# Optimization experiments

Hardware: AMD Instinct MI355X
Metric: run time of the kernel (lower is better)

## Reference

```python
import jax, jax.numpy as jnp
import numpy as np

M = N = 768
Q = 32
P_ROW = P_COL = 4
NB_ITER = 3


def cheb_basis(L, order):
    # Chebyshev polynomials T_k(L), stacked -> (order+1, n, n)
    n = L.shape[0]
    Ts = [jnp.eye(n, dtype=L.dtype)]
    if order > 0:
        Ts.append(L)
    for _ in range(2, order + 1):
        Ts.append(2.0 * (L @ Ts[-1]) - Ts[-2])
    return jnp.stack(Ts)


def setup_inputs() -> dict:
    key = jax.random.key(0)
    ks = jax.random.split(key, 24)
    f32 = jnp.float32
    # scaled symmetric Laplacians with small spectral radius (keeps Cheb recursion stable)
    Ar = jax.random.normal(ks[0], (M, M), dtype=f32)
    L_row = (Ar + Ar.T) / (2.0 * jnp.sqrt(jnp.float32(M)))
    Ac = jax.random.normal(ks[1], (N, N), dtype=f32)
    L_col = (Ac + Ac.T) / (2.0 * jnp.sqrt(jnp.float32(N)))
    x = jax.random.normal(ks[2], (M, N), dtype=f32)
    theta = 0.05 * jax.random.normal(ks[3], (P_ROW + 1, P_COL + 1, Q), dtype=f32)
    bias = jnp.zeros((Q,), dtype=f32)
    s = 1.0 / np.sqrt(Q)
    def w(k):
        return s * jax.random.normal(k, (Q, Q), dtype=f32)
    inp = {
        'x': x, 'L_row': L_row, 'L_col': L_col, 'theta': theta, 'bias': bias,
        'W_f': w(ks[4]), 'U_f': w(ks[5]), 'b_f': jnp.zeros((Q,), f32),
        'W_i': w(ks[6]), 'U_i': w(ks[7]), 'b_i': jnp.zeros((Q,), f32),
        'W_o': w(ks[8]), 'U_o': w(ks[9]), 'b_o': jnp.zeros((Q,), f32),
        'W_c': w(ks[10]), 'U_c': w(ks[11]), 'b_c': jnp.zeros((Q,), f32),
        'W_out': s * jax.random.normal(ks[12], (Q, 1), dtype=f32),
        'b_out': jnp.zeros((1, 1), f32),
        'nb_iterations_rnn': NB_ITER,
    }
    return inp


def reference(x, L_row, L_col, theta, bias,
              W_f, U_f, b_f, W_i, U_i, b_i, W_o, U_o, b_o, W_c, U_c, b_c,
              W_out, b_out, nb_iterations_rnn):
    pr = theta.shape[0] - 1
    pc = theta.shape[1] - 1
    q = theta.shape[2]
    m, n = x.shape
    Tr = cheb_basis(L_row, pr)  # (pr+1, M, M)
    Tc = cheb_basis(L_col, pc)  # (pc+1, N, N)

    def conv(xx):
        xr = jnp.einsum('imp,pn->imn', Tr, xx)            # (pr+1, M, N)
        bf = jnp.einsum('imn,jnk->ijmk', xr, Tc)           # (pr+1, pc+1, M, N)
        return jnp.einsum('ijmn,ijo->omn', bf, theta) + bias[:, None, None]

    def step(carry, _):
        xx, h, c = carry
        xc = conv(xx).transpose(1, 2, 0).reshape(-1, q)    # (M*N, q)
        f = jax.nn.sigmoid(xc @ W_f + h @ U_f + b_f)
        i = jax.nn.sigmoid(xc @ W_i + h @ U_i + b_i)
        o = jax.nn.sigmoid(xc @ W_o + h @ U_o + b_o)
        cu = jax.nn.sigmoid(xc @ W_c + h @ U_c + b_c)      # note: sigmoid, as in source
        c = f * c + i * cu
        h = o * jax.nn.sigmoid(c)                           # note: sigmoid(c), as in source
        dx = jnp.tanh(c @ W_out + b_out).reshape(m, n)
        return (xx + dx, h, c), None

    h0 = jnp.zeros((m * n, q), dtype=x.dtype)
    c0 = jnp.zeros((m * n, q), dtype=x.dtype)
    (x_out, _, _), _ = jax.lax.scan(step, (x, h0, c0), None, length=int(nb_iterations_rnn))
    return x_out
```

## Files before the change

kernel.cpp:

```cpp
#include <hip/hip_runtime.h>
#include <hip/hip_bf16.h>
#include <stdint.h>


#define DIM 768
#define MXK 589824
#define STK 2949120

typedef _Float16 f16x8 __attribute__((ext_vector_type(8)));
typedef float f32x4 __attribute__((ext_vector_type(4)));
typedef unsigned short ushort_t;
typedef _Float16 f16_t;

__device__ __forceinline__ float sigm(float v) {
    float e = __expf(-v);
    return __builtin_amdgcn_rcpf(1.0f + e);
}
__device__ __forceinline__ void split2h(float f, f16_t& h1, f16_t& h2) {
    h1 = (f16_t)f;
    h2 = (f16_t)(f - (float)h1);
}

__device__ __forceinline__ void gl_lds16(const f16_t* g, f16_t* l) {
    auto gp = reinterpret_cast<const __attribute__((address_space(1))) uint32_t*>(
        reinterpret_cast<uintptr_t>(g));
    auto lp = reinterpret_cast<__attribute__((address_space(3))) uint32_t*>(
        reinterpret_cast<uintptr_t>(l));
    __builtin_amdgcn_global_load_lds(gp, lp, 16, 0, 0);
}

__global__ __launch_bounds__(256) void init_split(
    const float* __restrict__ Lrow, const float* __restrict__ Lcol,
    f16_t* __restrict__ S0, f16_t* __restrict__ S1)
{
    int idx = blockIdx.x * 256 + threadIdx.x;
    int p = idx / DIM, m = idx % DIM;
    f16_t eye = (p == m) ? (f16_t)1.0f : (f16_t)0.0f;
    S0[idx] = eye; S1[idx] = (f16_t)0.0f;
    S0[STK + idx] = eye; S1[STK + idx] = (f16_t)0.0f;
    f16_t h1, h2;
    split2h(Lrow[idx], h1, h2);
    S0[MXK + idx] = h1; S1[MXK + idx] = h2;
    split2h(Lcol[idx], h1, h2);
    S0[STK + MXK + idx] = h1; S1[STK + MXK + idx] = h2;
}

__global__ __launch_bounds__(256) void prep_gate(
    const float* __restrict__ Wf, const float* __restrict__ Wi,
    const float* __restrict__ Wo, const float* __restrict__ Wc,
    const float* __restrict__ Uf, const float* __restrict__ Ui,
    const float* __restrict__ Uo, const float* __restrict__ Uc,
    const float* __restrict__ theta, const float* __restrict__ biasv,
    f16_t* __restrict__ Wstack, f16_t* __restrict__ thstack)
{
    int idx = blockIdx.x * 256 + threadIdx.x;
    if (idx < 8192) {
        int R = idx >> 6, k = idx & 63;
        int g = (R >> 4) & 3, o = (R >> 6) * 16 + (R & 15);
        const float* Wg[4] = {Wf, Wi, Wo, Wc};
        const float* Ug[4] = {Uf, Ui, Uo, Uc};
        float v = (k < 32) ? Wg[g][k * 32 + o] : Ug[g][(k - 32) * 32 + o];
        Wstack[idx] = (f16_t)v;
    } else if (idx < 9216) {
        int t = idx - 8192;
        int o = t >> 5, k = t & 31;
        float v = (k < 25) ? theta[k * 32 + o]
                           : (k == 25 ? biasv[o] : 0.0f);
        thstack[o * 32 + k] = (f16_t)v;
    }
}

__global__ __launch_bounds__(256) void transpose_cvt2x(
    const float* __restrict__ in, f16_t* __restrict__ o1,
    f16_t* __restrict__ o2, f16_t* __restrict__ xr0,
    f16_t* __restrict__ Cbf)
{
    __shared__ float t[32][33];
    int x = threadIdx.x & 31, y = threadIdx.x >> 5;
    int bx = blockIdx.x * 32, by = blockIdx.y * 32;
#pragma unroll
    for (int r = 0; r < 4; ++r) {
        int p = by + y + 8 * r, q = bx + x;
        size_t oi = (size_t)p * DIM + q;
        float v = in[oi];
        t[y + 8 * r][x] = v;
        f16_t hv = (f16_t)v;
        xr0[oi] = hv;
        Cbf[(size_t)p * 3840 + q] = hv;
    }
    __syncthreads();
#pragma unroll
    for (int r = 0; r < 4; ++r) {
        float v = t[x][y + 8 * r];
        f16_t h1, h2;
        split2h(v, h1, h2);
        size_t o = (size_t)(bx + y + 8 * r) * DIM + by + x;
        o1[o] = h1; o2[o] = h2;
    }
}

__global__ __launch_bounds__(256, 4) void gemm_bt_h2(
    const f16_t* __restrict__ A1,
    const f16_t* __restrict__ B1, const f16_t* __restrict__ B2,
    const f16_t* __restrict__ P1, const f16_t* __restrict__ P2,
    f16_t* __restrict__ D1, f16_t* __restrict__ D2, f16_t* __restrict__ D3,
    int K, int ldc, int mode, int nbx, int halfStride, int coloff)
{
    __shared__ __align__(16) f16_t sA[2][128 * 32];
    __shared__ __align__(16) f16_t sB[2][2 * 96 * 32];

    const int tid = threadIdx.x;

    int bx, by;
    size_t hoff = 0;
    int aoff = 0, boff = 0, poff = 0, doff = 0;
    if (mode == 3) {
        int g = blockIdx.x;
        int sup = g >> 8;
        int rows0 = sup * 8;
        int H = 30 - rows0; if (H > 8) H = 8;
        int local = g - rows0 * nbx;
        by = rows0 + local % H;
        bx = local / H;
    } else if (mode == 4) {
        int g = blockIdx.x;
        int t34 = g / 96, r = g % 96;
        int stack = r / 48, rr = r % 48;
        by = rr >> 3; bx = rr & 7;
        hoff = (size_t)stack * halfStride;
        if (t34 == 0) { aoff = MXK; boff = 2 * MXK; poff = MXK; doff = 3 * MXK; }
        else          { aoff = 2 * MXK; boff = 2 * MXK; poff = 0; doff = 4 * MXK; }
    } else {
        bx = blockIdx.x % nbx;
        by = blockIdx.x / nbx;
        if (mode == 2 && by >= 6) { by -= 6; hoff = (size_t)halfStride; }
    }
    const int m0 = by * 128, n0 = bx * 96;

    const f16_t* Asrc1 = A1 + hoff + aoff;
    const f16_t* Bsrc1 = B1 + hoff + boff;
    const f16_t* Bsrc2 = B2 + hoff + boff;
    const f16_t* Pq1 = P1 ? P1 + hoff + poff : nullptr;
    const f16_t* Pq2 = P2 ? P2 + hoff + poff : nullptr;
    f16_t* Dq1 = D1 + hoff + doff;
    f16_t* Dq2 = D2 ? D2 + hoff + doff : nullptr;

    const int lane = tid & 63, w4 = tid >> 6;
    const int wm = (w4 & 1) * 64, wn = (w4 >> 1) * 48;
    const int lm = lane & 15, quad = lane >> 4;
    const int psw = (quad ^ ((lm >> 1) & 3)) * 8;

    const f16_t* gApt[2]; int aslot[2];
#pragma unroll
    for (int cc = 0; cc < 2; ++cc) {
        int s = cc * 256 + w4 * 64 + lane;
        int row = s >> 2, pos = s & 3;
        int chunk = pos ^ ((row >> 1) & 3);
        gApt[cc] = Asrc1 + (size_t)(m0 + row) * K + chunk * 8;
        aslot[cc] = s * 8;
    }
    const f16_t* gBpt[3]; int bslot[3];
#pragma unroll
    for (int cc = 0; cc < 3; ++cc) {
        int slot = cc * 256 + w4 * 64 + lane;
        int lev = slot >= 384 ? 1 : 0;
        int s = slot - lev * 384;
        int row = s >> 2, pos = s & 3;
        int chunk = pos ^ ((row >> 1) & 3);
        gBpt[cc] = (lev ? Bsrc2 : Bsrc1) + (size_t)(n0 + row) * K + chunk * 8;
        bslot[cc] = lev * 3072 + s * 8;
    }

    f32x4 acc[4][3] = {};

#pragma unroll
    for (int cc = 0; cc < 2; ++cc) gl_lds16(gApt[cc], &sA[0][aslot[cc]]);
#pragma unroll
    for (int cc = 0; cc < 3; ++cc) gl_lds16(gBpt[cc], &sB[0][bslot[cc]]);
    __syncthreads();

    int ib = 0;
    for (int kb = 0; kb < K; kb += 32, ib ^= 1) {
        if (kb + 32 < K) {
            int nb = ib ^ 1;
#pragma unroll
            for (int cc = 0; cc < 2; ++cc)
                gl_lds16(gApt[cc] + kb + 32, &sA[nb][aslot[cc]]);
#pragma unroll
            for (int cc = 0; cc < 3; ++cc)
                gl_lds16(gBpt[cc] + kb + 32, &sB[nb][bslot[cc]]);
        }

        f16x8 bfr[2][3];
#pragma unroll
        for (int l = 0; l < 2; ++l)
#pragma unroll
            for (int fn = 0; fn < 3; ++fn)
                bfr[l][fn] = *(const f16x8*)&sB[ib][l * 3072 +
                                                (wn + fn * 16 + lm) * 32 + psw];
#pragma unroll
        for (int fm = 0; fm < 4; ++fm) {
            f16x8 a1v = *(const f16x8*)&sA[ib][(wm + fm * 16 + lm) * 32 + psw];
#pragma unroll
            for (int fn = 0; fn < 3; ++fn) {
                acc[fm][fn] = __builtin_amdgcn_mfma_f32_16x16x32_f16(
                    a1v, bfr[0][fn], acc[fm][fn], 0, 0, 0);
                acc[fm][fn] = __builtin_amdgcn_mfma_f32_16x16x32_f16(
                    a1v, bfr[1][fn], acc[fm][fn], 0, 0, 0);
            }
        }
        __syncthreads();
    }

#pragma unroll
    for (int fm = 0; fm < 4; ++fm)
#pragma unroll
        for (int fn = 0; fn < 3; ++fn) {
            int col = n0 + wn + fn * 16 + lm;
#pragma unroll
            for (int r = 0; r < 4; ++r) {
                int row = m0 + wm + fm * 16 + quad * 4 + r;
                float val = acc[fm][fn][r];
                if (mode == 3) {
                    Dq1[(size_t)row * ldc + coloff + col] = (f16_t)val;
                } else if (mode == 1) {
                    Dq1[(size_t)row * ldc + col] = (f16_t)val;
                    if (D3) D3[(size_t)row * 3840 + col] = (f16_t)val;
                } else {
                    size_t o = (size_t)row * ldc + col;
                    val = 2.0f * val - ((float)Pq1[o] + (float)Pq2[o]);
                    f16_t h1, h2;
                    split2h(val, h1, h2);
                    Dq1[o] = h1; Dq2[o] = h2;
                }
            }
        }
}

__global__ __launch_bounds__(256, 4) void gate_theta_mfma(
    const f16_t* __restrict__ Cbf, const f16_t* __restrict__ thstack,
    const f16_t* __restrict__ Wstack,
    const float* __restrict__ bfv, const float* __restrict__ biv,
    const float* __restrict__ bov, const float* __restrict__ bcv,
    const float* __restrict__ Wout, const float* __restrict__ bout,
    f16_t* __restrict__ h, f16_t* __restrict__ c, float* __restrict__ x,
    int first, int last)
{
    __shared__ __align__(16) ushort_t sB[128 * 40];
    __shared__ __align__(16) ushort_t sC[26 * 128];
    __shared__ float red[256];

    const int tid = threadIdx.x;
    const int lane = tid & 63, w4 = tid >> 6;
    const int wm = (w4 & 1) * 64, wn = (w4 >> 1) * 64;
    const int lm = lane & 15, quad = lane >> 4;
    const int m = blockIdx.x / 6;
    const int n0 = (blockIdx.x % 6) * 128;
    const int pbase = m * DIM + n0;
    const int o0 = (wm >> 2) + quad * 4;

#pragma unroll
    for (int cc = 0; cc < 2; ++cc) {
        int s = cc * 256 + tid;
        if (s < 416) {
            int ij = s >> 4, f = s & 15;
            if (ij < 25) {
                int i5 = (ij * 205) >> 10;
                int j5 = ij - i5 * 5;
                size_t ga = (size_t)(i5 * DIM + m) * 3840 + j5 * DIM + n0 + f * 8;
                *(uint4*)&sC[ij * 128 + f * 8] = *(const uint4*)&Cbf[ga];
            } else {
                uint4 ones;
                ones.x = ones.y = ones.z = ones.w = 0x3C003C00u;
                *(uint4*)&sC[25 * 128 + f * 8] = ones;
            }
        }
    }

    f16x8 bth[2];
#pragma unroll
    for (int fn = 0; fn < 2; ++fn)
        bth[fn] = *(const f16x8*)&thstack[(fn * 16 + lm) * 32 + quad * 8];

    f16x8 hfr[4];
    f16_t cold[4][4];
    if (!first) {
#pragma unroll
        for (int fn = 0; fn < 4; ++fn) {
            size_t p = (size_t)(pbase + wn + fn * 16 + lm);
            hfr[fn] = *(const f16x8*)&h[p * 32 + quad * 8];
            *(uint2*)cold[fn] = *(const uint2*)&c[p * 32 + o0];
        }
    } else {
#pragma unroll
        for (int fn = 0; fn < 4; ++fn) {
#pragma unroll
            for (int j = 0; j < 8; ++j) hfr[fn][j] = (f16_t)0.0f;
#pragma unroll
            for (int r = 0; r < 4; ++r) cold[fn][r] = (f16_t)0.0f;
        }
    }

    __syncthreads();

    {
        const f16_t* sCf = (const f16_t*)sC;
        const int pw = w4 * 32;
        f32x4 tacc[2][2] = {};
        f16x8 a0, a1;
#pragma unroll
        for (int j = 0; j < 8; ++j) {
            int k = quad * 8 + j;
            int ij = k > 25 ? 25 : k;
            a0[j] = sCf[ij * 128 + pw + lm];
            a1[j] = sCf[ij * 128 + pw + 16 + lm];
        }
#pragma unroll
        for (int fn = 0; fn < 2; ++fn) {
            tacc[0][fn] = __builtin_amdgcn_mfma_f32_16x16x32_f16(
                a0, bth[fn], tacc[0][fn], 0, 0, 0);
            tacc[1][fn] = __builtin_amdgcn_mfma_f32_16x16x32_f16(
                a1, bth[fn], tacc[1][fn], 0, 0, 0);
        }
#pragma unroll
        for (int fm2 = 0; fm2 < 2; ++fm2)
#pragma unroll
            for (int fn = 0; fn < 2; ++fn)
#pragma unroll
                for (int r = 0; r < 4; ++r) {
                    f16_t hv = (f16_t)tacc[fm2][fn][r];
                    sB[(pw + fm2 * 16 + quad * 4 + r) * 40 + fn * 16 + lm] =
                        __builtin_bit_cast(ushort_t, hv);
                }
    }

    f16x8 af[4][2];
#pragma unroll
    for (int fm = 0; fm < 4; ++fm)
#pragma unroll
        for (int kc = 0; kc < 2; ++kc)
            af[fm][kc] = *(const f16x8*)&Wstack[(wm + fm * 16 + lm) * 64 +
                                                kc * 32 + quad * 8];
    __syncthreads();

    const float4 bgf = *(const float4*)&bfv[o0];
    const float4 bgi = *(const float4*)&biv[o0];
    const float4 bgo = *(const float4*)&bov[o0];
    const float4 bgc = *(const float4*)&bcv[o0];
    const float4 wo4 = *(const float4*)&Wout[o0];
    float bf4[4] = {bgf.x, bgf.y, bgf.z, bgf.w};
    float bi4[4] = {bgi.x, bgi.y, bgi.z, bgi.w};
    float bo4[4] = {bgo.x, bgo.y, bgo.z, bgo.w};
    float bc4[4] = {bgc.x, bgc.y, bgc.z, bgc.w};
    float wo[4] = {wo4.x, wo4.y, wo4.z, wo4.w};

#pragma unroll
    for (int fn = 0; fn < 4; ++fn) {
        f16x8 bxc = *(const f16x8*)&sB[(wn + fn * 16 + lm) * 40 + quad * 8];
        f32x4 acc[4] = {};
#pragma unroll
        for (int fm = 0; fm < 4; ++fm) {
            acc[fm] = __builtin_amdgcn_mfma_f32_16x16x32_f16(
                af[fm][0], bxc, acc[fm], 0, 0, 0);
            acc[fm] = __builtin_amdgcn_mfma_f32_16x16x32_f16(
                af[fm][1], hfr[fn], acc[fm], 0, 0, 0);
        }

        int px = wn + fn * 16 + lm;
        size_t p = (size_t)(pbase + px);
        f16_t cn16[4], hn16[4];
        float part = 0.f;
#pragma unroll
        for (int r = 0; r < 4; ++r) {
            float fg = sigm(acc[0][r] + bf4[r]);
            float ig = sigm(acc[1][r] + bi4[r]);
            float og = sigm(acc[2][r] + bo4[r]);
            float gg = sigm(acc[3][r] + bc4[r]);
            float cn = fg * (float)cold[fn][r] + ig * gg;
            cn16[r] = (f16_t)cn;
            hn16[r] = (f16_t)(og * sigm(cn));
            part = fmaf(cn, wo[r], part);
        }
        if (!last) {
            *(uint2*)&c[p * 32 + o0] = *(const uint2*)cn16;
            *(uint2*)&h[p * 32 + o0] = *(const uint2*)hn16;
        }
        part += __shfl_xor(part, 16, 64);
        part += __shfl_xor(part, 32, 64);
        if (quad == 0) red[px * 2 + (wm >> 6)] = part;
    }
    __syncthreads();
    if (tid < 128) {
        float v = red[tid * 2] + red[tid * 2 + 1] + bout[0];
        v = fminf(fmaxf(v, -15.f), 15.f);
        float e = __expf(2.f * v);
        x[pbase + tid] += (e - 1.f) * __builtin_amdgcn_rcpf(e + 1.f);
    }
}

extern "C" void kernel_launch(void* const* d_in, const int* in_sizes, int n_in,
                              void* d_out, int out_size, void* d_ws, size_t ws_size,
                              hipStream_t stream)
{
    const float* x_in  = (const float*)d_in[0];
    const float* Lrow  = (const float*)d_in[1];
    const float* Lcol  = (const float*)d_in[2];
    const float* theta = (const float*)d_in[3];
    const float* bias  = (const float*)d_in[4];
    const float* Wf = (const float*)d_in[5];
    const float* Uf = (const float*)d_in[6];
    const float* bf = (const float*)d_in[7];
    const float* Wi = (const float*)d_in[8];
    const float* Ui = (const float*)d_in[9];
    const float* bi = (const float*)d_in[10];
    const float* Wo = (const float*)d_in[11];
    const float* Uo = (const float*)d_in[12];
    const float* bo = (const float*)d_in[13];
    const float* Wc = (const float*)d_in[14];
    const float* Uc = (const float*)d_in[15];
    const float* bc = (const float*)d_in[16];
    const float* Wout = (const float*)d_in[17];
    const float* bout = (const float*)d_in[18];
    (void)in_sizes; (void)n_in; (void)out_size;

    float* out = (float*)d_out;

    f16_t* base = (f16_t*)d_ws;
    f16_t* Cbf  = base;
    f16_t* h    = Cbf + 14745600;
    f16_t* c    = h + 18874368;
    f16_t* S0   = c + 18874368;
    f16_t* S1   = S0 + 2 * STK;
    f16_t* XR0  = S1 + 2 * STK;
    f16_t* Wstack  = XR0 + STK;
    f16_t* thstack = Wstack + 8192;
    f16_t* xT0  = thstack + 1024;
    f16_t* xT1  = xT0 + MXK;
    if (ws_size < (size_t)136857600) return;

    hipMemcpyAsync(out, x_in, (size_t)MXK * 4, hipMemcpyDeviceToDevice, stream);

    prep_gate<<<36, 256, 0, stream>>>(Wf, Wi, Wo, Wc, Uf, Ui, Uo, Uc, theta,
                                      bias, Wstack, thstack);
    init_split<<<MXK / 256, 256, 0, stream>>>(Lrow, Lcol, S0, S1);
    gemm_bt_h2<<<96, 256, 0, stream>>>(
        S0 + MXK, S0 + MXK, S1 + MXK, S0, S1,
        S0 + 2 * MXK, S1 + 2 * MXK, nullptr,
        DIM, DIM, 2, 8, STK, 0);
    gemm_bt_h2<<<192, 256, 0, stream>>>(
        S0, S0, S1, S0, S1, S0, S1, nullptr,
        DIM, DIM, 4, 8, STK, 0);

    for (int it = 0; it < 3; ++it) {
        transpose_cvt2x<<<dim3(24, 24), 256, 0, stream>>>(out, xT0, xT1,
                                                          XR0, Cbf);
        gemm_bt_h2<<<192, 256, 0, stream>>>(
            S0 + MXK, xT0, xT1,
            nullptr, nullptr,
            XR0 + MXK, nullptr, Cbf + (size_t)DIM * 3840,
            DIM, DIM, 1, 8, 0, 0);
        gemm_bt_h2<<<960, 256, 0, stream>>>(
            XR0, S0 + STK + MXK, S1 + STK + MXK,
            nullptr, nullptr,
            Cbf, nullptr, nullptr, DIM, 3840, 3, 32, 0, DIM);
        gate_theta_mfma<<<4608, 256, 0, stream>>>(
            Cbf, thstack, Wstack,
            bf, bi, bo, bc, Wout, bout, h, c, out,
            it == 0 ? 1 : 0, it == 2 ? 1 : 0);
    }
}
```

Baseline: 509.4 us.

## Make gate kernel persistent per row with double-buffered async staging

```diff
diff --git a/kernel.cpp b/kernel.cpp
--- a/kernel.cpp
+++ b/kernel.cpp
@@ -237,7 +237,7 @@
         }
 }
 
-__global__ __launch_bounds__(256, 4) void gate_theta_mfma(
+__global__ __launch_bounds__(256, 3) void gate_theta_mfma(
     const f16_t* __restrict__ Cbf, const f16_t* __restrict__ thstack,
     const f16_t* __restrict__ Wstack,
     const float* __restrict__ bfv, const float* __restrict__ biv,
@@ -246,94 +246,42 @@
     f16_t* __restrict__ h, f16_t* __restrict__ c, float* __restrict__ x,
     int first, int last)
 {
-    __shared__ __align__(16) ushort_t sB[128 * 40];
-    __shared__ __align__(16) ushort_t sC[26 * 128];
+    __shared__ __align__(16) ushort_t sC[2][26 * 128];
+    __shared__ __align__(16) ushort_t sB[2][128 * 40];
     __shared__ float red[256];
 
     const int tid = threadIdx.x;
     const int lane = tid & 63, w4 = tid >> 6;
     const int wm = (w4 & 1) * 64, wn = (w4 >> 1) * 64;
     const int lm = lane & 15, quad = lane >> 4;
-    const int m = blockIdx.x / 6;
-    const int n0 = (blockIdx.x % 6) * 128;
-    const int pbase = m * DIM + n0;
+    const int m = blockIdx.x;
     const int o0 = (wm >> 2) + quad * 4;
-
-#pragma unroll
-    for (int cc = 0; cc < 2; ++cc) {
-        int s = cc * 256 + tid;
-        if (s < 416) {
-            int ij = s >> 4, f = s & 15;
-            if (ij < 25) {
+    const int pw = w4 * 32;
+
+    if (tid < 32) {
+        uint4 ones;
+        ones.x = ones.y = ones.z = ones.w = 0x3C003C00u;
+        *(uint4*)&sC[tid >> 4][25 * 128 + (tid & 15) * 8] = ones;
+    }
+
+    auto stage = [&](int n0, int buf) {
+#pragma unroll
+        for (int cc = 0; cc < 2; ++cc) {
+            int s = cc * 256 + tid;
+            if (s < 400) {
+                int ij = s >> 4, f = s & 15;
                 int i5 = (ij * 205) >> 10;
                 int j5 = ij - i5 * 5;
                 size_t ga = (size_t)(i5 * DIM + m) * 3840 + j5 * DIM + n0 + f * 8;
-                *(uint4*)&sC[ij * 128 + f * 8] = *(const uint4*)&Cbf[ga];
-            } else {
-                uint4 ones;
-                ones.x = ones.y = ones.z = ones.w = 0x3C003C00u;
-                *(uint4*)&sC[25 * 128 + f * 8] = ones;
-            }
-        }
-    }
+                gl_lds16(&Cbf[ga], (f16_t*)&sC[buf][ij * 128 + f * 8]);
+            }
+        }
+    };
 
     f16x8 bth[2];
 #pragma unroll
     for (int fn = 0; fn < 2; ++fn)
         bth[fn] = *(const f16x8*)&thstack[(fn * 16 + lm) * 32 + quad * 8];
-
-    f16x8 hfr[4];
-    f16_t cold[4][4];
-    if (!first) {
-#pragma unroll
-        for (int fn = 0; fn < 4; ++fn) {
-            size_t p = (size_t)(pbase + wn + fn * 16 + lm);
-            hfr[fn] = *(const f16x8*)&h[p * 32 + quad * 8];
-            *(uint2*)cold[fn] = *(const uint2*)&c[p * 32 + o0];
-        }
-    } else {
-#pragma unroll
-        for (int fn = 0; fn < 4; ++fn) {
-#pragma unroll
-            for (int j = 0; j < 8; ++j) hfr[fn][j] = (f16_t)0.0f;
-#pragma unroll
-            for (int r = 0; r < 4; ++r) cold[fn][r] = (f16_t)0.0f;
-        }
-    }
-
-    __syncthreads();
-
-    {
-        const f16_t* sCf = (const f16_t*)sC;
-        const int pw = w4 * 32;
-        f32x4 tacc[2][2] = {};
-        f16x8 a0, a1;
-#pragma unroll
-        for (int j = 0; j < 8; ++j) {
-            int k = quad * 8 + j;
-            int ij = k > 25 ? 25 : k;
-            a0[j] = sCf[ij * 128 + pw + lm];
-            a1[j] = sCf[ij * 128 + pw + 16 + lm];
-        }
-#pragma unroll
-        for (int fn = 0; fn < 2; ++fn) {
-            tacc[0][fn] = __builtin_amdgcn_mfma_f32_16x16x32_f16(
-                a0, bth[fn], tacc[0][fn], 0, 0, 0);
-            tacc[1][fn] = __builtin_amdgcn_mfma_f32_16x16x32_f16(
-                a1, bth[fn], tacc[1][fn], 0, 0, 0);
-        }
-#pragma unroll
-        for (int fm2 = 0; fm2 < 2; ++fm2)
-#pragma unroll
-            for (int fn = 0; fn < 2; ++fn)
-#pragma unroll
-                for (int r = 0; r < 4; ++r) {
-                    f16_t hv = (f16_t)tacc[fm2][fn][r];
-                    sB[(pw + fm2 * 16 + quad * 4 + r) * 40 + fn * 16 + lm] =
-                        __builtin_bit_cast(ushort_t, hv);
-                }
-    }
-
     f16x8 af[4][2];
 #pragma unroll
     for (int fm = 0; fm < 4; ++fm)
@@ -341,8 +289,6 @@
         for (int kc = 0; kc < 2; ++kc)
             af[fm][kc] = *(const f16x8*)&Wstack[(wm + fm * 16 + lm) * 64 +
                                                 kc * 32 + quad * 8];
-    __syncthreads();
-
     const float4 bgf = *(const float4*)&bfv[o0];
     const float4 bgi = *(const float4*)&biv[o0];
     const float4 bgo = *(const float4*)&bov[o0];
@@ -353,48 +299,136 @@
     float bo4[4] = {bgo.x, bgo.y, bgo.z, bgo.w};
     float bc4[4] = {bgc.x, bgc.y, bgc.z, bgc.w};
     float wo[4] = {wo4.x, wo4.y, wo4.z, wo4.w};
-
-#pragma unroll
-    for (int fn = 0; fn < 4; ++fn) {
-        f16x8 bxc = *(const f16x8*)&sB[(wn + fn * 16 + lm) * 40 + quad * 8];
-        f32x4 acc[4] = {};
-#pragma unroll
-        for (int fm = 0; fm < 4; ++fm) {
-            acc[fm] = __builtin_amdgcn_mfma_f32_16x16x32_f16(
-                af[fm][0], bxc, acc[fm], 0, 0, 0);
-            acc[fm] = __builtin_amdgcn_mfma_f32_16x16x32_f16(
-                af[fm][1], hfr[fn], acc[fm], 0, 0, 0);
-        }
-
-        int px = wn + fn * 16 + lm;
-        size_t p = (size_t)(pbase + px);
-        f16_t cn16[4], hn16[4];
-        float part = 0.f;
-#pragma unroll
-        for (int r = 0; r < 4; ++r) {
-            float fg = sigm(acc[0][r] + bf4[r]);
-            float ig = sigm(acc[1][r] + bi4[r]);
-            float og = sigm(acc[2][r] + bo4[r]);
-            float gg = sigm(acc[3][r] + bc4[r]);
-            float cn = fg * (float)cold[fn][r] + ig * gg;
-            cn16[r] = (f16_t)cn;
-            hn16[r] = (f16_t)(og * sigm(cn));
-            part = fmaf(cn, wo[r], part);
-        }
-        if (!last) {
-            *(uint2*)&c[p * 32 + o0] = *(const uint2*)cn16;
-            *(uint2*)&h[p * 32 + o0] = *(const uint2*)hn16;
-        }
-        part += __shfl_xor(part, 16, 64);
-        part += __shfl_xor(part, 32, 64);
-        if (quad == 0) red[px * 2 + (wm >> 6)] = part;
+    const float bout0 = bout[0];
+
+    stage(0, 0);
+    f16x8 hfr[4];
+    f16_t cold[4][4];
+    if (!first) {
+#pragma unroll
+        for (int fn = 0; fn < 4; ++fn) {
+            size_t p = (size_t)(m * DIM + wn + fn * 16 + lm);
+            hfr[fn] = *(const f16x8*)&h[p * 32 + quad * 8];
+            *(uint2*)cold[fn] = *(const uint2*)&c[p * 32 + o0];
+        }
+    } else {
+#pragma unroll
+        for (int fn = 0; fn < 4; ++fn) {
+#pragma unroll
+            for (int j = 0; j < 8; ++j) hfr[fn][j] = (f16_t)0.0f;
+#pragma unroll
+            for (int r = 0; r < 4; ++r) cold[fn][r] = (f16_t)0.0f;
+        }
     }
     __syncthreads();
-    if (tid < 128) {
-        float v = red[tid * 2] + red[tid * 2 + 1] + bout[0];
-        v = fminf(fmaxf(v, -15.f), 15.f);
-        float e = __expf(2.f * v);
-        x[pbase + tid] += (e - 1.f) * __builtin_amdgcn_rcpf(e + 1.f);
+
+    int tb = 0;
+    for (int t = 0; t < 6; ++t, tb ^= 1) {
+        const int n0 = t * 128;
+        const int pbase = m * DIM + n0;
+
+        {
+            const f16_t* sCf = (const f16_t*)sC[tb];
+            f32x4 tacc[2][2] = {};
+            f16x8 a0, a1;
+#pragma unroll
+            for (int j = 0; j < 8; ++j) {
+                int k = quad * 8 + j;
+                int ij = k > 25 ? 25 : k;
+                a0[j] = sCf[ij * 128 + pw + lm];
+                a1[j] = sCf[ij * 128 + pw + 16 + lm];
+            }
+#pragma unroll
+            for (int fn = 0; fn < 2; ++fn) {
+                tacc[0][fn] = __builtin_amdgcn_mfma_f32_16x16x32_f16(
+                    a0, bth[fn], tacc[0][fn], 0, 0, 0);
+                tacc[1][fn] = __builtin_amdgcn_mfma_f32_16x16x32_f16(
+                    a1, bth[fn], tacc[1][fn], 0, 0, 0);
+            }
+#pragma unroll
+            for (int fm2 = 0; fm2 < 2; ++fm2)
+#pragma unroll
+                for (int fn = 0; fn < 2; ++fn)
+#pragma unroll
+                    for (int r = 0; r < 4; ++r) {
+                        f16_t hv = (f16_t)tacc[fm2][fn][r];
+                        sB[tb][(pw + fm2 * 16 + quad * 4 + r) * 40 +
+                               fn * 16 + lm] = __builtin_bit_cast(ushort_t, hv);
+                    }
+        }
+        __syncthreads();
+
+        if (t < 5) stage(n0 + 128, tb ^ 1);
+        f16x8 hfrn[4];
+        f16_t coldn[4][4];
+        if (t < 5 && !first) {
+#pragma unroll
+            for (int fn = 0; fn < 4; ++fn) {
+                size_t p = (size_t)(pbase + 128 + wn + fn * 16 + lm);
+                hfrn[fn] = *(const f16x8*)&h[p * 32 + quad * 8];
+                *(uint2*)coldn[fn] = *(const uint2*)&c[p * 32 + o0];
+            }
+        } else {
+#pragma unroll
+            for (int fn = 0; fn < 4; ++fn) {
+#pragma unroll
+                for (int j = 0; j < 8; ++j) hfrn[fn][j] = (f16_t)0.0f;
+#pragma unroll
+                for (int r = 0; r < 4; ++r) coldn[fn][r] = (f16_t)0.0f;
+            }
+        }
+
+#pragma unroll
+        for (int fn = 0; fn < 4; ++fn) {
+            f16x8 bxc = *(const f16x8*)&sB[tb][(wn + fn * 16 + lm) * 40 +
+                                              quad * 8];
+            f32x4 acc[4] = {};
+#pragma unroll
+            for (int fm = 0; fm < 4; ++fm) {
+                acc[fm] = __builtin_amdgcn_mfma_f32_16x16x32_f16(
+                    af[fm][0], bxc, acc[fm], 0, 0, 0);
+                acc[fm] = __builtin_amdgcn_mfma_f32_16x16x32_f16(
+                    af[fm][1], hfr[fn], acc[fm], 0, 0, 0);
+            }
+
+            int px = wn + fn * 16 + lm;
+            size_t p = (size_t)(pbase + px);
+            f16_t cn16[4], hn16[4];
+            float part = 0.f;
+#pragma unroll
+            for (int r = 0; r < 4; ++r) {
+                float fg = sigm(acc[0][r] + bf4[r]);
+                float ig = sigm(acc[1][r] + bi4[r]);
+                float og = sigm(acc[2][r] + bo4[r]);
+                float gg = sigm(acc[3][r] + bc4[r]);
+                float cn = fg * (float)cold[fn][r] + ig * gg;
+                cn16[r] = (f16_t)cn;
+                hn16[r] = (f16_t)(og * sigm(cn));
+                part = fmaf(cn, wo[r], part);
+            }
+            if (!last) {
+                *(uint2*)&c[p * 32 + o0] = *(const uint2*)cn16;
+                *(uint2*)&h[p * 32 + o0] = *(const uint2*)hn16;
+            }
+            part += __shfl_xor(part, 16, 64);
+            part += __shfl_xor(part, 32, 64);
+            if (quad == 0) red[px * 2 + (wm >> 6)] = part;
+        }
+        __syncthreads();
+
+        if (tid < 128) {
+            float v = red[tid * 2] + red[tid * 2 + 1] + bout0;
+            v = fminf(fmaxf(v, -15.f), 15.f);
+            float e = __expf(2.f * v);
+            x[pbase + tid] += (e - 1.f) * __builtin_amdgcn_rcpf(e + 1.f);
+        }
+
+#pragma unroll
+        for (int fn = 0; fn < 4; ++fn) {
+            hfr[fn] = hfrn[fn];
+#pragma unroll
+            for (int r = 0; r < 4; ++r) cold[fn][r] = coldn[fn][r];
+        }
     }
 }
 
@@ -463,7 +497,7 @@
             XR0, S0 + STK + MXK, S1 + STK + MXK,
             nullptr, nullptr,
             Cbf, nullptr, nullptr, DIM, 3840, 3, 32, 0, DIM);
-        gate_theta_mfma<<<4608, 256, 0, stream>>>(
+        gate_theta_mfma<<<768, 256, 0, stream>>>(
             Cbf, thstack, Wstack,
             bf, bi, bo, bc, Wout, bout, h, c, out,
             it == 0 ? 1 : 0, it == 2 ? 1 : 0);
```

Result: faster. 486.0 us (-4.6%).
